# Kernel optimization log

Measured on AMD Instinct MI355X. Metric: run time of the kernel, lower is better.

Reference implementation:

```python
import jax, jax.numpy as jnp
import numpy as np

EPS = 1e-3    # Keras BatchNormalization default epsilon
ALPHA = 0.3   # Keras LeakyReLU default negative slope


def _bn(x, axes):
    # BatchNormalization(center=False, scale=False) in training mode: batch stats
    m = jnp.mean(x, axis=axes, keepdims=True)
    v = jnp.var(x, axis=axes, keepdims=True)
    return (x - m) * jax.lax.rsqrt(v + EPS)


def _leaky(x):
    return jnp.where(x > 0, x, ALPHA * x)


def setup_inputs() -> dict:
    key = jax.random.key(0)
    ks = jax.random.split(key, 8)
    B, A, D, Hid, H, hd = 8192, 16, 256, 512, 8, 64
    s = 0.02
    return {
        "state": jax.random.normal(ks[0], (B, A, D), jnp.float32),
        "agent_index": 3,
        "Ws": jax.random.normal(ks[1], (D, Hid), jnp.float32) * s,
        "bs": jnp.zeros((Hid,), jnp.float32),
        "Wc": jax.random.normal(ks[2], (D, Hid), jnp.float32) * s,
        "bc": jnp.zeros((Hid,), jnp.float32),
        "Wk": jax.random.normal(ks[3], (H, Hid, hd), jnp.float32) * s,
        "Wq": jax.random.normal(ks[4], (H, Hid, hd), jnp.float32) * s,
        "Wv": jax.random.normal(ks[5], (H, Hid, hd), jnp.float32) * s,
    }


def reference(state, agent_index, Ws, bs, Wc, bc, Wk, Wq, Wv):
    B = state.shape[0]
    H, _, hd = Wk.shape
    ai = int(agent_index)

    # current agent encoder: BN over batch, Dense, LeakyReLU -> [B, Hid]
    cur = state[:, ai, :]
    s_enc = _leaky(_bn(cur, (0,)) @ Ws + bs)

    # other agents encoder: BN over (batch, agent), Dense, LeakyReLU -> [B, A-1, Hid]
    others = jnp.concatenate([state[:, :ai, :], state[:, ai + 1:, :]], axis=1)
    sa_enc = _leaky(_bn(others, (0, 1)) @ Wc + bc)

    # batched per-head projections (replaces the python loop over heads)
    k = jnp.einsum('ban,hnd->bhad', sa_enc, Wk)           # [B,H,A-1,hd]
    v = _leaky(jnp.einsum('ban,hnd->bhad', sa_enc, Wv))   # [B,H,A-1,hd]
    q = jnp.einsum('bn,hnd->bhd', s_enc, Wq)              # [B,H,hd]

    scores = jnp.einsum('bhd,bhad->bha', q, k) / jnp.sqrt(jnp.float32(hd))
    w = jax.nn.softmax(scores, axis=-1)                   # [B,H,A-1]
    att = jnp.einsum('bha,bhad->bhd', w, v)               # [B,H,hd]

    # concat heads in order -> [B, H*hd]
    return att.reshape(B, H * hd)
```

## Files before the change

kernel.cpp:

```cpp
#include <hip/hip_runtime.h>
#include <hip/hip_bf16.h>

typedef __attribute__((ext_vector_type(8))) short short8;
typedef __attribute__((ext_vector_type(8))) unsigned short ushort8;
typedef __attribute__((ext_vector_type(4))) unsigned short bfu4;
typedef __attribute__((ext_vector_type(4))) float f32x4;

__device__ __forceinline__ unsigned short f2bf(float f){
  return __builtin_bit_cast(unsigned short, __float2bfloat16(f));
}
__device__ __forceinline__ float bf2f(unsigned short h){
  unsigned int u = ((unsigned int)h) << 16;
  return __builtin_bit_cast(float, u);
}
__device__ __forceinline__ float leaky(float x){ return x > 0.f ? x : 0.3f * x; }

__global__ __launch_bounds__(1024) void ca_stats_prep(const float* __restrict__ state,
    const int* __restrict__ agp, float* __restrict__ part, int B,
    const float* __restrict__ Wk, const float* __restrict__ Wv, const float* __restrict__ Wq,
    unsigned short* __restrict__ WkT, unsigned short* __restrict__ WvT,
    unsigned short* __restrict__ WqT, unsigned short* __restrict__ WkF2,
    unsigned short* __restrict__ WvF, unsigned short* __restrict__ WqF, int writeT){
  __shared__ f32x4 red[16][4][64];
  if (blockIdx.x < 256){
    int q = threadIdx.x & 63, sl = threadIdx.x >> 6;
    int ag = agp[0];
    int bPer = (B + 255) >> 8;
    int b0 = blockIdx.x * bPer;
    f32x4 zero4 = {0.f,0.f,0.f,0.f};
    f32x4 sC = zero4, ssC = zero4, sO = zero4, ssO = zero4;
    for (int b = sl; b < bPer; b += 16){
      int bb = b0 + b;
      if (bb >= B) continue;
      const float* row = state + ((size_t)bb << 12) + q*4;
      #pragma unroll
      for (int a = 0; a < 16; a++){
        f32x4 v = *(const f32x4*)(row + a*256);
        f32x4 vv = v * v;
        if (a == ag){ sC += v; ssC += vv; } else { sO += v; ssO += vv; }
      }
    }
    red[sl][0][q] = sC; red[sl][1][q] = ssC; red[sl][2][q] = sO; red[sl][3][q] = ssO;
    __syncthreads();
    if (threadIdx.x < 256){
      int st = threadIdx.x >> 6, qq = threadIdx.x & 63;
      f32x4 s = red[0][st][qq];
      #pragma unroll
      for (int g = 1; g < 16; g++) s += red[g][st][qq];
      *(f32x4*)(part + (size_t)blockIdx.x*1024 + st*256 + qq*4) = s;
    }
    return;
  }
  int bid2 = blockIdx.x - 256;
  int m = bid2 >> 8;
  int c = ((bid2 & 255) << 1) | (threadIdx.x >> 9);
  int n = threadIdx.x & 511;
  if (m == 3){
    size_t idx = (size_t)c*512 + n;
    int h = (int)(idx >> 15), nn = (int)((idx >> 6) & 511), dd = (int)(idx & 63);
    int nt = nn >> 4, j = nn & 15, kq = dd >> 5, hi = (dd >> 3) & 3, e = dd & 7;
    WkF2[(size_t)((h*32 + nt)*2 + kq)*512 + (hi*16 + j)*8 + e] = f2bf(Wk[idx]);
    return;
  }
  if (m == 0 && !writeT) return;
  int h = c >> 6, dd = c & 63;
  const float* W = (m == 0) ? Wk : (m == 1) ? Wv : Wq;
  unsigned short* O = (m == 0) ? WkT : (m == 1) ? WvT : WqT;
  float scale = (m == 2) ? 0.125f : 1.f;
  unsigned short v = f2bf(W[((size_t)h*512 + n)*64 + dd] * scale);
  if (m == 0 || writeT) O[(size_t)c*512 + n] = v;
  if (m != 0){
    int nt = (c >> 4) & 3, j = c & 15;
    int kk = n >> 5, hi = (n >> 3) & 3, e = n & 7;
    size_t fi = (size_t)((h*16 + kk)*4 + nt)*512 + (hi*16 + j)*8 + e;
    if (m == 1) WvF[fi] = v; else WqF[fi] = v;
  }
}

__global__ __launch_bounds__(1024) void ca_stats_final(const float* __restrict__ part,
    float* __restrict__ stats, int nblk, int B){
  int dl = threadIdx.x & 63, sl = threadIdx.x >> 6;
  int d = blockIdx.x*64 + dl;
  float sC = 0.f, ssC = 0.f, sO = 0.f, ssO = 0.f;
  for (int g = sl; g < nblk; g += 16){
    const float* p = part + (size_t)g * 1024;
    sC += p[d]; ssC += p[d+256]; sO += p[d+512]; ssO += p[d+768];
  }
  __shared__ float red[16][4][64];
  red[sl][0][dl] = sC; red[sl][1][dl] = ssC; red[sl][2][dl] = sO; red[sl][3][dl] = ssO;
  __syncthreads();
  if (sl == 0){
    sC = 0.f; ssC = 0.f; sO = 0.f; ssO = 0.f;
    #pragma unroll
    for (int g = 0; g < 16; g++){
      sC += red[g][0][dl]; ssC += red[g][1][dl]; sO += red[g][2][dl]; ssO += red[g][3][dl];
    }
    float nC = (float)B, nO = (float)B * 15.f;
    float mC = sC / nC, vC = ssC / nC - mC * mC;
    float mO = sO / nO, vO = ssO / nO - mO * mO;
    float rC = rsqrtf(vC + 1e-3f), rO = rsqrtf(vO + 1e-3f);
    stats[d] = rC; stats[d+256] = mC * rC; stats[d+512] = rO; stats[d+768] = mO * rO;
  }
}

__global__ __launch_bounds__(256) void ca_prep_sc(const float* __restrict__ Ws,
    const float* __restrict__ bs, const float* __restrict__ Wc, const float* __restrict__ bc,
    const float* __restrict__ stats, unsigned short* __restrict__ WsT,
    unsigned short* __restrict__ WcT, unsigned short* __restrict__ WsF,
    unsigned short* __restrict__ WcF, float* __restrict__ bsp, float* __restrict__ bcp,
    int writeT){
  int n = blockIdx.x, d = threadIdx.x;
  float rC = stats[d], mrC = stats[d+256], rO = stats[d+512], mrO = stats[d+768];
  float ws = Ws[(size_t)d*512 + n], wc = Wc[(size_t)d*512 + n];
  unsigned short wsb = f2bf(ws * rC), wcb = f2bf(wc * rO);
  if (writeT){
    WsT[(size_t)n*256 + d] = wsb;
    WcT[(size_t)n*256 + d] = wcb;
  }
  {
    int h = n >> 6, nt = (n >> 4) & 3, j = n & 15;
    int kk = d >> 5, hi = (d >> 3) & 3, e = d & 7;
    size_t fi = (size_t)((h*8 + kk)*4 + nt)*512 + (hi*16 + j)*8 + e;
    WsF[fi] = wsb;
    WcF[fi] = wcb;
  }
  __shared__ float red[256];
  red[d] = mrC * ws;
  __syncthreads();
  for (int s = 128; s > 0; s >>= 1){ if (d < s) red[d] += red[d+s]; __syncthreads(); }
  if (d == 0) bsp[n] = bs[n] - red[0];
  __syncthreads();
  red[d] = mrO * wc;
  __syncthreads();
  for (int s = 128; s > 0; s >>= 1){ if (d < s) red[d] += red[d+s]; __syncthreads(); }
  if (d == 0) bcp[n] = bc[n] - red[0];
}

__global__ __launch_bounds__(512) void ca_prep_kvq(const float* __restrict__ Wk,
    const float* __restrict__ Wv, const float* __restrict__ Wq,
    unsigned short* __restrict__ WkT, unsigned short* __restrict__ WvT,
    unsigned short* __restrict__ WqT){
  int c = blockIdx.x & 511, m = blockIdx.x >> 9;
  int n = threadIdx.x;
  int h = c >> 6, dd = c & 63;
  const float* W = (m == 0) ? Wk : (m == 1) ? Wv : Wq;
  unsigned short* O = (m == 0) ? WkT : (m == 1) ? WvT : WqT;
  float scale = (m == 2) ? 0.125f : 1.f;
  O[(size_t)c*512 + n] = f2bf(W[((size_t)h*512 + n)*64 + dd] * scale);
}

__global__ __launch_bounds__(512) void ca_q_kernel(const float* __restrict__ state,
    const int* __restrict__ agp,
    const unsigned short* __restrict__ WsT, const float* __restrict__ bsp,
    const unsigned short* __restrict__ WqT, unsigned short* __restrict__ Qws){
  __shared__ unsigned short U[32*512];
  __shared__ float bias_s[512];
  unsigned short* Alds = U;
  unsigned short* SE = U;
  int tid = threadIdx.x, lane = tid & 63, w = tid >> 6;
  int j = lane & 15, hi = lane >> 4;
  int b0 = blockIdx.x * 32;
  int ag = agp[0];

  for (int s = tid; s < 32*32; s += 512){
    int row = s >> 5, kg = s & 31;
    const float* p = state + (((size_t)(b0 + row) * 16 + ag) << 8) + kg * 8;
    f32x4 v0 = *(const f32x4*)p, v1 = *(const f32x4*)(p + 4);
    ushort8 hv;
    hv[0]=f2bf(v0[0]); hv[1]=f2bf(v0[1]); hv[2]=f2bf(v0[2]); hv[3]=f2bf(v0[3]);
    hv[4]=f2bf(v1[0]); hv[5]=f2bf(v1[1]); hv[6]=f2bf(v1[2]); hv[7]=f2bf(v1[3]);
    *(ushort8*)&Alds[row*256 + ((kg ^ (row & 7)) << 3)] = hv;
  }
  bias_s[tid & 511] = bsp[tid & 511];
  __syncthreads();

  int cb = w * 64;
  f32x4 zero4 = {0.f, 0.f, 0.f, 0.f};
  f32x4 acc[2][4];
  #pragma unroll
  for (int a1 = 0; a1 < 2; a1++)
    #pragma unroll
    for (int a2 = 0; a2 < 4; a2++) acc[a1][a2] = zero4;

  #pragma unroll
  for (int kk = 0; kk < 8; kk++){
    short8 bfr[4];
    #pragma unroll
    for (int nt = 0; nt < 4; nt++)
      bfr[nt] = *(const short8*)&WsT[(size_t)(cb + nt*16 + j)*256 + kk*32 + hi*8];
    #pragma unroll
    for (int mt = 0; mt < 2; mt++){
      int row = mt*16 + j;
      short8 afr = *(const short8*)&Alds[row*256 + ((((kk << 2) | hi) ^ (row & 7)) << 3)];
      #pragma unroll
      for (int nt = 0; nt < 4; nt++)
        acc[mt][nt] = __builtin_amdgcn_mfma_f32_16x16x32_bf16(afr, bfr[nt], acc[mt][nt], 0, 0, 0);
    }
  }
  __syncthreads();
  #pragma unroll
  for (int mt = 0; mt < 2; mt++)
    #pragma unroll
    for (int nt = 0; nt < 4; nt++)
      #pragma unroll
      for (int i = 0; i < 4; i++){
        int row = mt*16 + hi*4 + i, col = cb + nt*16 + j;
        float x = leaky(acc[mt][nt][i] + bias_s[col]);
        SE[row*512 + ((((col >> 3) ^ (row & 7)) << 3) | (col & 7))] = f2bf(x);
      }
  __syncthreads();

  f32x4 qa[2][4];
  #pragma unroll
  for (int a1 = 0; a1 < 2; a1++)
    #pragma unroll
    for (int a2 = 0; a2 < 4; a2++) qa[a1][a2] = zero4;
  #pragma unroll
  for (int kk = 0; kk < 16; kk++){
    short8 bfr[4];
    #pragma unroll
    for (int nt = 0; nt < 4; nt++)
      bfr[nt] = *(const short8*)&WqT[(size_t)(cb + nt*16 + j)*512 + kk*32 + hi*8];
    #pragma unroll
    for (int mt = 0; mt < 2; mt++){
      int row = mt*16 + j;
      short8 afr = *(const short8*)&SE[row*512 + ((((kk << 2) | hi) ^ (row & 7)) << 3)];
      #pragma unroll
      for (int nt = 0; nt < 4; nt++)
        qa[mt][nt] = __builtin_amdgcn_mfma_f32_16x16x32_bf16(afr, bfr[nt], qa[mt][nt], 0, 0, 0);
    }
  }
  #pragma unroll
  for (int mt = 0; mt < 2; mt++)
    #pragma unroll
    for (int nt = 0; nt < 4; nt++)
      #pragma unroll
      for (int i = 0; i < 4; i++)
        Qws[(size_t)(b0 + mt*16 + hi*4 + i)*512 + cb + nt*16 + j] = f2bf(qa[mt][nt][i]);
}

__global__ __launch_bounds__(1024) void ca_q_kernel_qk(const float* __restrict__ state,
    const int* __restrict__ agp,
    const unsigned short* __restrict__ WsF, const float* __restrict__ bsp,
    const unsigned short* __restrict__ WqF, const unsigned short* __restrict__ WkF2,
    unsigned short* __restrict__ QKws){
  __shared__ unsigned short U[2][16*512];
  __shared__ float bias_s[512];
  int tid = threadIdx.x, lane = tid & 63, w = tid >> 6;
  int g16 = w >> 3, wl = w & 7;
  int j = lane & 15, hi = lane >> 4;
  int b0 = blockIdx.x * 32 + g16 * 16;
  int ag = agp[0];
  f32x4 zero4 = {0.f, 0.f, 0.f, 0.f};
  unsigned short* Alds = U[g16];
  unsigned short* SE = U[g16];
  unsigned short* Qlds = U[g16];
  int sub = tid & 511;

  {
    int row = sub >> 5, kg = sub & 31;
    const float* p = state + (((size_t)(b0 + row) * 16 + ag) << 8) + kg * 8;
    f32x4 v0 = *(const f32x4*)p, v1 = *(const f32x4*)(p + 4);
    ushort8 hv;
    hv[0]=f2bf(v0[0]); hv[1]=f2bf(v0[1]); hv[2]=f2bf(v0[2]); hv[3]=f2bf(v0[3]);
    hv[4]=f2bf(v1[0]); hv[5]=f2bf(v1[1]); hv[6]=f2bf(v1[2]); hv[7]=f2bf(v1[3]);
    *(ushort8*)&Alds[row*256 + ((kg ^ (row & 7)) << 3)] = hv;
  }
  if (tid < 512) bias_s[tid] = bsp[tid];
  __syncthreads();

  int cb = wl * 64;

  f32x4 acc[4];
  #pragma unroll
  for (int a2 = 0; a2 < 4; a2++) acc[a2] = zero4;
  #pragma unroll
  for (int kk = 0; kk < 8; kk++){
    short8 bfr[4];
    #pragma unroll
    for (int nt = 0; nt < 4; nt++)
      bfr[nt] = *(const short8*)&WsF[(size_t)((wl*8 + kk)*4 + nt)*512 + lane*8];
    short8 afr = *(const short8*)&Alds[j*256 + ((((kk << 2) | hi) ^ (j & 7)) << 3)];
    #pragma unroll
    for (int nt = 0; nt < 4; nt++)
      acc[nt] = __builtin_amdgcn_mfma_f32_16x16x32_bf16(bfr[nt], afr, acc[nt], 0, 0, 0);
  }
  __syncthreads();
  #pragma unroll
  for (int nt = 0; nt < 4; nt++){
    int nb = cb + nt*16 + hi*4;
    int g = nb >> 3;
    bfu4 pk;
    #pragma unroll
    for (int i = 0; i < 4; i++) pk[i] = f2bf(leaky(acc[nt][i] + bias_s[nb + i]));
    *(bfu4*)&SE[j*512 + ((g ^ (j & 7)) << 3) + (hi & 1)*4] = pk;
  }
  __syncthreads();

  f32x4 qa[4];
  #pragma unroll
  for (int a2 = 0; a2 < 4; a2++) qa[a2] = zero4;
  #pragma unroll
  for (int kk = 0; kk < 16; kk++){
    short8 bfr[4];
    #pragma unroll
    for (int nt = 0; nt < 4; nt++)
      bfr[nt] = *(const short8*)&WqF[(size_t)((wl*16 + kk)*4 + nt)*512 + lane*8];
    short8 afr = *(const short8*)&SE[j*512 + ((((kk << 2) | hi) ^ (j & 7)) << 3)];
    #pragma unroll
    for (int nt = 0; nt < 4; nt++)
      qa[nt] = __builtin_amdgcn_mfma_f32_16x16x32_bf16(bfr[nt], afr, qa[nt], 0, 0, 0);
  }
  __syncthreads();
  #pragma unroll
  for (int nt = 0; nt < 4; nt++){
    int nb = cb + nt*16 + hi*4;
    int g = nb >> 3;
    bfu4 pk;
    #pragma unroll
    for (int i = 0; i < 4; i++) pk[i] = f2bf(qa[nt][i]);
    *(bfu4*)&Qlds[j*512 + ((g ^ (j & 7)) << 3) + (hi & 1)*4] = pk;
  }
  __syncthreads();

  short8 aq[2];
  #pragma unroll
  for (int kq = 0; kq < 2; kq++){
    int gq = wl*8 + kq*4 + hi;
    aq[kq] = *(const short8*)&Qlds[j*512 + ((gq ^ (j & 7)) << 3)];
  }
  for (int nt = 0; nt < 32; nt++){
    short8 bf0 = *(const short8*)&WkF2[(size_t)((wl*32 + nt)*2 + 0)*512 + lane*8];
    short8 bf1 = *(const short8*)&WkF2[(size_t)((wl*32 + nt)*2 + 1)*512 + lane*8];
    f32x4 qt = zero4;
    qt = __builtin_amdgcn_mfma_f32_16x16x32_bf16(bf0, aq[0], qt, 0, 0, 0);
    qt = __builtin_amdgcn_mfma_f32_16x16x32_bf16(bf1, aq[1], qt, 0, 0, 0);
    bfu4 pk;
    pk[0] = f2bf(qt[0]); pk[1] = f2bf(qt[1]); pk[2] = f2bf(qt[2]); pk[3] = f2bf(qt[3]);
    *(bfu4*)&QKws[((size_t)(b0 + j)*8 + wl)*512 + nt*16 + hi*4] = pk;
  }
}

__global__ __launch_bounds__(512) void ca_main_kernel_qk(const float* __restrict__ state,
    const int* __restrict__ agp,
    const unsigned short* __restrict__ WcF, const float* __restrict__ bcp,
    const unsigned short* __restrict__ WvF, const unsigned short* __restrict__ QKws,
    float* __restrict__ out){
  __shared__ unsigned short U[128*512];
  __shared__ float bias_s[512];
  __shared__ float Wl[8*16*8];
  unsigned short* Alds = U;
  unsigned short* SA = U;
  int tid = threadIdx.x, lane = tid & 63, w = tid >> 6;
  int j = lane & 15, hi = lane >> 4;
  int b0 = blockIdx.x * 8;
  int ag = agp[0];
  f32x4 zero4 = {0.f, 0.f, 0.f, 0.f};
  short8 zero8 = {0,0,0,0,0,0,0,0};

  #pragma unroll
  for (int g = 0; g < 2; g++){
    f32x4 st0[4], st1[4];
    #pragma unroll
    for (int it = 0; it < 4; it++){
      int s = tid + 512*(g*4 + it);
      int row = s >> 5, kg = s & 31;
      int bl = row >> 4, ai = row & 15;
      if (ai < 15){
        int a = ai + (ai >= ag ? 1 : 0);
        const float* p = state + (((size_t)(b0 + bl) * 16 + a) << 8) + kg * 8;
        st0[it] = *(const f32x4*)p;
        st1[it] = *(const f32x4*)(p + 4);
      } else { st0[it] = zero4; st1[it] = zero4; }
    }
    #pragma unroll
    for (int it = 0; it < 4; it++){
      int s = tid + 512*(g*4 + it);
      int row = s >> 5, kg = s & 31;
      ushort8 hv;
      hv[0]=f2bf(st0[it][0]); hv[1]=f2bf(st0[it][1]); hv[2]=f2bf(st0[it][2]); hv[3]=f2bf(st0[it][3]);
      hv[4]=f2bf(st1[it][0]); hv[5]=f2bf(st1[it][1]); hv[6]=f2bf(st1[it][2]); hv[7]=f2bf(st1[it][3]);
      *(ushort8*)&Alds[row*256 + ((kg ^ (row & 7)) << 3)] = hv;
    }
  }
  bias_s[tid] = bcp[tid];
  __syncthreads();

  int cb = w * 64;

  f32x4 acc[8][4];
  #pragma unroll
  for (int a1 = 0; a1 < 8; a1++)
    #pragma unroll
    for (int a2 = 0; a2 < 4; a2++) acc[a1][a2] = zero4;
  {
    short8 bcur[4], bnxt[4];
    #pragma unroll
    for (int nt = 0; nt < 4; nt++)
      bcur[nt] = *(const short8*)&WcF[(size_t)((w*8 + 0)*4 + nt)*512 + lane*8];
    #pragma unroll 2
    for (int kk = 0; kk < 8; kk++){
      if (kk < 7){
        #pragma unroll
        for (int nt = 0; nt < 4; nt++)
          bnxt[nt] = *(const short8*)&WcF[(size_t)((w*8 + kk + 1)*4 + nt)*512 + lane*8];
      }
      #pragma unroll
      for (int mt = 0; mt < 8; mt++){
        int row = mt*16 + j;
        short8 afr = *(const short8*)&Alds[row*256 + ((((kk << 2) | hi) ^ (row & 7)) << 3)];
        #pragma unroll
        for (int nt = 0; nt < 4; nt++)
          acc[mt][nt] = __builtin_amdgcn_mfma_f32_16x16x32_bf16(bcur[nt], afr, acc[mt][nt], 0, 0, 0);
      }
      #pragma unroll
      for (int nt = 0; nt < 4; nt++) bcur[nt] = bnxt[nt];
    }
  }
  __syncthreads();
  #pragma unroll
  for (int mt = 0; mt < 8; mt++)
    #pragma unroll
    for (int nt = 0; nt < 4; nt++){
      int m = mt*16 + j;
      int nb = cb + nt*16 + hi*4;
      int g = nb >> 3;
      bfu4 pk;
      #pragma unroll
      for (int i = 0; i < 4; i++) pk[i] = f2bf(leaky(acc[mt][nt][i] + bias_s[nb + i]));
      *(bfu4*)&SA[m*512 + ((g ^ (m & 7)) << 3) + (hi & 1)*4] = pk;
    }
  __syncthreads();

  f32x4 qs = zero4;
  {
    size_t qbase = ((size_t)(b0 + w)*8 + (j & 7))*512;
    #pragma unroll
    for (int kk = 0; kk < 16; kk++){
      short8 bq = *(const short8*)&QKws[qbase + kk*32 + hi*8];
      if (j >= 8) bq = zero8;
      int row = w*16 + j;
      short8 afr = *(const short8*)&SA[row*512 + ((((kk << 2) | hi) ^ (row & 7)) << 3)];
      qs = __builtin_amdgcn_mfma_f32_16x16x32_bf16(afr, bq, qs, 0, 0, 0);
    }
  }
  {
    float sv0 = qs[0], sv1 = qs[1], sv2 = qs[2], sv3 = qs[3];
    sv3 = (hi == 3) ? -1e30f : sv3;
    float m = fmaxf(fmaxf(sv0, sv1), fmaxf(sv2, sv3));
    m = fmaxf(m, __shfl_xor(m, 16)); m = fmaxf(m, __shfl_xor(m, 32));
    float e0 = __expf(sv0-m), e1 = __expf(sv1-m), e2 = __expf(sv2-m), e3 = __expf(sv3-m);
    float sum = e0 + e1 + e2 + e3;
    sum += __shfl_xor(sum, 16); sum += __shfl_xor(sum, 32);
    float inv = 1.f / sum;
    if (j < 8){
      Wl[w*128 + (hi*4+0)*8 + j] = e0*inv;
      Wl[w*128 + (hi*4+1)*8 + j] = e1*inv;
      Wl[w*128 + (hi*4+2)*8 + j] = e2*inv;
      Wl[w*128 + (hi*4+3)*8 + j] = e3*inv;
    }
  }

  f32x4 va[8][4];
  #pragma unroll
  for (int a1 = 0; a1 < 8; a1++)
    #pragma unroll
    for (int a2 = 0; a2 < 4; a2++) va[a1][a2] = zero4;
  {
    short8 bcur[4], bnxt[4];
    #pragma unroll
    for (int nt = 0; nt < 4; nt++)
      bcur[nt] = *(const short8*)&WvF[(size_t)((w*16 + 0)*4 + nt)*512 + lane*8];
    #pragma unroll 2
    for (int kk = 0; kk < 16; kk++){
      if (kk < 15){
        #pragma unroll
        for (int nt = 0; nt < 4; nt++)
          bnxt[nt] = *(const short8*)&WvF[(size_t)((w*16 + kk + 1)*4 + nt)*512 + lane*8];
      }
      #pragma unroll
      for (int mt = 0; mt < 8; mt++){
        int row = mt*16 + j;
        short8 afr = *(const short8*)&SA[row*512 + ((((kk << 2) | hi) ^ (row & 7)) << 3)];
        #pragma unroll
        for (int nt = 0; nt < 4; nt++)
          va[mt][nt] = __builtin_amdgcn_mfma_f32_16x16x32_bf16(afr, bcur[nt], va[mt][nt], 0, 0, 0);
      }
      #pragma unroll
      for (int nt = 0; nt < 4; nt++) bcur[nt] = bnxt[nt];
    }
  }
  __syncthreads();

  #pragma unroll
  for (int mt = 0; mt < 8; mt++){
    float w0 = Wl[mt*128 + (hi*4+0)*8 + w];
    float w1 = Wl[mt*128 + (hi*4+1)*8 + w];
    float w2 = Wl[mt*128 + (hi*4+2)*8 + w];
    float w3 = Wl[mt*128 + (hi*4+3)*8 + w];
    float ap0 = w0*leaky(va[mt][0][0]) + w1*leaky(va[mt][0][1]) + w2*leaky(va[mt][0][2]) + w3*leaky(va[mt][0][3]);
    float ap1 = w0*leaky(va[mt][1][0]) + w1*leaky(va[mt][1][1]) + w2*leaky(va[mt][1][2]) + w3*leaky(va[mt][1][3]);
    float ap2 = w0*leaky(va[mt][2][0]) + w1*leaky(va[mt][2][1]) + w2*leaky(va[mt][2][2]) + w3*leaky(va[mt][2][3]);
    float ap3 = w0*leaky(va[mt][3][0]) + w1*leaky(va[mt][3][1]) + w2*leaky(va[mt][3][2]) + w3*leaky(va[mt][3][3]);
    ap0 += __shfl_xor(ap0, 16); ap0 += __shfl_xor(ap0, 32);
    ap1 += __shfl_xor(ap1, 16); ap1 += __shfl_xor(ap1, 32);
    ap2 += __shfl_xor(ap2, 16); ap2 += __shfl_xor(ap2, 32);
    ap3 += __shfl_xor(ap3, 16); ap3 += __shfl_xor(ap3, 32);
    float val = (hi == 0) ? ap0 : (hi == 1) ? ap1 : (hi == 2) ? ap2 : ap3;
    out[(size_t)(b0 + mt)*512 + cb + lane] = val;
  }
}

__global__ __launch_bounds__(512) void ca_main_kernel(const float* __restrict__ state,
    const int* __restrict__ agp,
    const unsigned short* __restrict__ WcT, const float* __restrict__ bcp,
    const unsigned short* __restrict__ WkT, const unsigned short* __restrict__ WvT,
    const unsigned short* __restrict__ Qws, float* __restrict__ out){
  __shared__ unsigned short U[128*512];
  __shared__ unsigned short Qs[8*512];
  __shared__ float bias_s[512];
  unsigned short* Alds = U;
  unsigned short* SA = U;
  int tid = threadIdx.x, lane = tid & 63, w = tid >> 6;
  int j = lane & 15, hi = lane >> 4;
  int b0 = blockIdx.x * 8;
  int ag = agp[0];
  f32x4 zero4 = {0.f, 0.f, 0.f, 0.f};

  #pragma unroll
  for (int g = 0; g < 2; g++){
    f32x4 st0[4], st1[4];
    #pragma unroll
    for (int it = 0; it < 4; it++){
      int s = tid + 512*(g*4 + it);
      int row = s >> 5, kg = s & 31;
      int bl = row >> 4, ai = row & 15;
      if (ai < 15){
        int a = ai + (ai >= ag ? 1 : 0);
        const float* p = state + (((size_t)(b0 + bl) * 16 + a) << 8) + kg * 8;
        st0[it] = *(const f32x4*)p;
        st1[it] = *(const f32x4*)(p + 4);
      } else { st0[it] = zero4; st1[it] = zero4; }
    }
    #pragma unroll
    for (int it = 0; it < 4; it++){
      int s = tid + 512*(g*4 + it);
      int row = s >> 5, kg = s & 31;
      ushort8 hv;
      hv[0]=f2bf(st0[it][0]); hv[1]=f2bf(st0[it][1]); hv[2]=f2bf(st0[it][2]); hv[3]=f2bf(st0[it][3]);
      hv[4]=f2bf(st1[it][0]); hv[5]=f2bf(st1[it][1]); hv[6]=f2bf(st1[it][2]); hv[7]=f2bf(st1[it][3]);
      *(ushort8*)&Alds[row*256 + ((kg ^ (row & 7)) << 3)] = hv;
    }
  }
  *(ushort8*)&Qs[tid*8] = *(const ushort8*)&Qws[(size_t)b0*512 + tid*8];
  bias_s[tid] = bcp[tid];
  __syncthreads();

  int cb = w * 64;

  f32x4 acc[8][4];
  #pragma unroll
  for (int a1 = 0; a1 < 8; a1++)
    #pragma unroll
    for (int a2 = 0; a2 < 4; a2++) acc[a1][a2] = zero4;
  {
    short8 bcur[4], bnxt[4];
    #pragma unroll
    for (int nt = 0; nt < 4; nt++)
      bcur[nt] = *(const short8*)&WcT[(size_t)(cb + nt*16 + j)*256 + hi*8];
    #pragma unroll 1
    for (int kk = 0; kk < 8; kk++){
      if (kk < 7){
        #pragma unroll
        for (int nt = 0; nt < 4; nt++)
          bnxt[nt] = *(const short8*)&WcT[(size_t)(cb + nt*16 + j)*256 + (kk+1)*32 + hi*8];
      }
      #pragma unroll
      for (int mt = 0; mt < 8; mt++){
        int row = mt*16 + j;
        short8 afr = *(const short8*)&Alds[row*256 + ((((kk << 2) | hi) ^ (row & 7)) << 3)];
        #pragma unroll
        for (int nt = 0; nt < 4; nt++)
          acc[mt][nt] = __builtin_amdgcn_mfma_f32_16x16x32_bf16(afr, bcur[nt], acc[mt][nt], 0, 0, 0);
      }
      #pragma unroll
      for (int nt = 0; nt < 4; nt++) bcur[nt] = bnxt[nt];
    }
  }
  __syncthreads();
  #pragma unroll
  for (int mt = 0; mt < 8; mt++)
    #pragma unroll
    for (int nt = 0; nt < 4; nt++)
      #pragma unroll
      for (int i = 0; i < 4; i++){
        int row = mt*16 + hi*4 + i, col = cb + nt*16 + j;
        float x = leaky(acc[mt][nt][i] + bias_s[col]);
        SA[row*512 + ((((col >> 3) ^ (row & 7)) << 3) | (col & 7))] = f2bf(x);
      }
  __syncthreads();

  f32x4 ka[8][4];
  #pragma unroll
  for (int a1 = 0; a1 < 8; a1++)
    #pragma unroll
    for (int a2 = 0; a2 < 4; a2++) ka[a1][a2] = zero4;
  {
    short8 bcur[4], bnxt[4];
    #pragma unroll
    for (int nt = 0; nt < 4; nt++)
      bcur[nt] = *(const short8*)&WkT[(size_t)(cb + nt*16 + j)*512 + hi*8];
    #pragma unroll 1
    for (int kk = 0; kk < 16; kk++){
      if (kk < 15){
        #pragma unroll
        for (int nt = 0; nt < 4; nt++)
          bnxt[nt] = *(const short8*)&WkT[(size_t)(cb + nt*16 + j)*512 + (kk+1)*32 + hi*8];
      }
      #pragma unroll
      for (int mt = 0; mt < 8; mt++){
        int row = mt*16 + j;
        short8 afr = *(const short8*)&SA[row*512 + ((((kk << 2) | hi) ^ (row & 7)) << 3)];
        #pragma unroll
        for (int nt = 0; nt < 4; nt++)
          ka[mt][nt] = __builtin_amdgcn_mfma_f32_16x16x32_bf16(afr, bcur[nt], ka[mt][nt], 0, 0, 0);
      }
      #pragma unroll
      for (int nt = 0; nt < 4; nt++) bcur[nt] = bnxt[nt];
    }
  }

  float wgt[8][4];
  #pragma unroll
  for (int mt = 0; mt < 8; mt++){
    float sv[4];
    #pragma unroll
    for (int i = 0; i < 4; i++){
      float t = 0.f;
      #pragma unroll
      for (int nt = 0; nt < 4; nt++)
        t += bf2f(Qs[mt*512 + cb + nt*16 + j]) * ka[mt][nt][i];
      t += __shfl_xor(t, 1); t += __shfl_xor(t, 2);
      t += __shfl_xor(t, 4); t += __shfl_xor(t, 8);
      sv[i] = t;
    }
    sv[3] = (hi == 3) ? -1e30f : sv[3];
    float m = fmaxf(fmaxf(sv[0], sv[1]), fmaxf(sv[2], sv[3]));
    m = fmaxf(m, __shfl_xor(m, 16)); m = fmaxf(m, __shfl_xor(m, 32));
    float e0 = __expf(sv[0]-m), e1 = __expf(sv[1]-m), e2 = __expf(sv[2]-m), e3 = __expf(sv[3]-m);
    float sum = e0 + e1 + e2 + e3;
    sum += __shfl_xor(sum, 16); sum += __shfl_xor(sum, 32);
    float inv = 1.f / sum;
    wgt[mt][0] = e0*inv; wgt[mt][1] = e1*inv; wgt[mt][2] = e2*inv; wgt[mt][3] = e3*inv;
  }

  f32x4 va[8][4];
  #pragma unroll
  for (int a1 = 0; a1 < 8; a1++)
    #pragma unroll
    for (int a2 = 0; a2 < 4; a2++) va[a1][a2] = zero4;
  {
    short8 bcur[4], bnxt[4];
    #pragma unroll
    for (int nt = 0; nt < 4; nt++)
      bcur[nt] = *(const short8*)&WvT[(size_t)(cb + nt*16 + j)*512 + hi*8];
    #pragma unroll 1
    for (int kk = 0; kk < 16; kk++){
      if (kk < 15){
        #pragma unroll
        for (int nt = 0; nt < 4; nt++)
          bnxt[nt] = *(const short8*)&WvT[(size_t)(cb + nt*16 + j)*512 + (kk+1)*32 + hi*8];
      }
      #pragma unroll
      for (int mt = 0; mt < 8; mt++){
        int row = mt*16 + j;
        short8 afr = *(const short8*)&SA[row*512 + ((((kk << 2) | hi) ^ (row & 7)) << 3)];
        #pragma unroll
        for (int nt = 0; nt < 4; nt++)
          va[mt][nt] = __builtin_amdgcn_mfma_f32_16x16x32_bf16(afr, bcur[nt], va[mt][nt], 0, 0, 0);
      }
      #pragma unroll
      for (int nt = 0; nt < 4; nt++) bcur[nt] = bnxt[nt];
    }
  }

  #pragma unroll
  for (int mt = 0; mt < 8; mt++){
    float ap0 = 0.f, ap1 = 0.f, ap2 = 0.f, ap3 = 0.f;
    #pragma unroll
    for (int i = 0; i < 4; i++){
      float wv = wgt[mt][i];
      ap0 += wv * leaky(va[mt][0][i]);
      ap1 += wv * leaky(va[mt][1][i]);
      ap2 += wv * leaky(va[mt][2][i]);
      ap3 += wv * leaky(va[mt][3][i]);
    }
    ap0 += __shfl_xor(ap0, 16); ap0 += __shfl_xor(ap0, 32);
    ap1 += __shfl_xor(ap1, 16); ap1 += __shfl_xor(ap1, 32);
    ap2 += __shfl_xor(ap2, 16); ap2 += __shfl_xor(ap2, 32);
    ap3 += __shfl_xor(ap3, 16); ap3 += __shfl_xor(ap3, 32);
    float val = (hi == 0) ? ap0 : (hi == 1) ? ap1 : (hi == 2) ? ap2 : ap3;
    out[(size_t)(b0 + mt)*512 + cb + lane] = val;
  }
}

extern "C" void kernel_launch(void* const* d_in, const int* in_sizes, int n_in,
                              void* d_out, int out_size, void* d_ws, size_t ws_size,
                              hipStream_t stream) {
  const float* state = (const float*)d_in[0];
  const int*   agp   = (const int*)d_in[1];
  const float* Ws    = (const float*)d_in[2];
  const float* bs    = (const float*)d_in[3];
  const float* Wc    = (const float*)d_in[4];
  const float* bc    = (const float*)d_in[5];
  const float* Wk    = (const float*)d_in[6];
  const float* Wq    = (const float*)d_in[7];
  const float* Wv    = (const float*)d_in[8];
  float* out = (float*)d_out;
  int B = in_sizes[0] / 4096;

  char* wsb = (char*)d_ws;
  float* part  = (float*)wsb;
  float* stats = (float*)(wsb + (1 << 20));
  float* bsp   = (float*)(wsb + (1 << 20) + 4096);
  float* bcp   = (float*)(wsb + (1 << 20) + 6144);
  unsigned short* WsT  = (unsigned short*)(wsb + (1 << 20) + 8192);
  unsigned short* WcT  = WsT  + 512*256;
  unsigned short* WkT  = WcT  + 512*256;
  unsigned short* WvT  = WkT  + 512*512;
  unsigned short* WqT  = WvT  + 512*512;
  unsigned short* WkF2 = WqT  + 512*512;
  unsigned short* Qws  = WkF2 + 512*512;
  unsigned short* QKws = Qws  + (size_t)B*512;
  unsigned short* WsF  = Qws;
  unsigned short* WcF  = WsF + 512*256;
  unsigned short* WqF  = WcF + 512*256;
  unsigned short* WvF  = WqF + 512*512;

  size_t need = ((size_t)(1 << 20) + 8192)
              + 2ull*(512*256 + 512*256 + 512*512 + 512*512 + 512*512 + 512*512)
              + 2ull*B*512 + 2ull*B*8*512;
  bool qkp = (ws_size >= need);
  int writeT = qkp ? 0 : 1;

  hipLaunchKernelGGL(ca_stats_prep, dim3(1280), dim3(1024), 0, stream, state, agp, part, B,
                     Wk, Wv, Wq, WkT, WvT, WqT, WkF2, WvF, WqF, writeT);
  hipLaunchKernelGGL(ca_stats_final, dim3(4), dim3(1024), 0, stream, part, stats, 256, B);
  hipLaunchKernelGGL(ca_prep_sc,     dim3(512), dim3(256), 0, stream, Ws, bs, Wc, bc, stats, WsT, WcT, WsF, WcF, bsp, bcp, writeT);
  if (qkp){
    hipLaunchKernelGGL(ca_q_kernel_qk,   dim3(B/32),dim3(1024), 0, stream, state, agp, WsF, bsp, WqF, WkF2, QKws);
    hipLaunchKernelGGL(ca_main_kernel_qk,dim3(B/8), dim3(512), 0, stream, state, agp, WcF, bcp, WvF, QKws, out);
  } else {
    hipLaunchKernelGGL(ca_prep_kvq,      dim3(1536),dim3(512), 0, stream, Wk, Wv, Wq, WkT, WvT, WqT);
    hipLaunchKernelGGL(ca_q_kernel,      dim3(B/32),dim3(512), 0, stream, state, agp, WsT, bsp, WqT, Qws);
    hipLaunchKernelGGL(ca_main_kernel,   dim3(B/8), dim3(512), 0, stream, state, agp, WcT, bcp, WkT, WvT, Qws, out);
  }
}
```

Baseline: 215.1 us.

## Apply batch-norm on activations in consumers and drop weight-folding prep launch

Batch-norm is no longer folded into the Ws/Wc weights and biases by a separate prep kernel. The q and main kernels now normalize state rows in registers from the stats buffer while converting to bf16, and use the raw biases. Packing Ws/Wc into the fragment layout moves into the stats kernel's spare blocks, so it runs alongside the reduction and one dependent launch leaves the fast path. The main kernel also loads its QK fragments before the barrier to hide global latency. The cost is a few extra FMAs per loaded element and bf16 rounding applied to the normalized inputs rather than to the folded weights.

```diff
diff --git a/kernel.cpp b/kernel.cpp
--- a/kernel.cpp
+++ b/kernel.cpp
@@ -18,9 +18,10 @@
 __global__ __launch_bounds__(1024) void ca_stats_prep(const float* __restrict__ state,
     const int* __restrict__ agp, float* __restrict__ part, int B,
     const float* __restrict__ Wk, const float* __restrict__ Wv, const float* __restrict__ Wq,
-    unsigned short* __restrict__ WkT, unsigned short* __restrict__ WvT,
-    unsigned short* __restrict__ WqT, unsigned short* __restrict__ WkF2,
-    unsigned short* __restrict__ WvF, unsigned short* __restrict__ WqF, int writeT){
+    const float* __restrict__ Ws, const float* __restrict__ Wc,
+    unsigned short* __restrict__ WkF2, unsigned short* __restrict__ WvF,
+    unsigned short* __restrict__ WqF, unsigned short* __restrict__ WsF,
+    unsigned short* __restrict__ WcF){
   __shared__ f32x4 red[16][4][64];
   if (blockIdx.x < 256){
     int q = threadIdx.x & 63, sl = threadIdx.x >> 6;
@@ -53,28 +54,34 @@
   }
   int bid2 = blockIdx.x - 256;
   int m = bid2 >> 8;
+  if (m == 3){
+    int item = ((bid2 & 255) << 10) | threadIdx.x;
+    const float* W = (item < 131072) ? Ws : Wc;
+    unsigned short* O = (item < 131072) ? WsF : WcF;
+    int it2 = item & 131071;
+    int n = it2 >> 8, d = it2 & 255;
+    int h = n >> 6, nt = (n >> 4) & 3, j = n & 15;
+    int kk = d >> 5, hi = (d >> 3) & 3, e = d & 7;
+    O[(size_t)((h*8 + kk)*4 + nt)*512 + (hi*16 + j)*8 + e] = f2bf(W[(size_t)d*512 + n]);
+    return;
+  }
   int c = ((bid2 & 255) << 1) | (threadIdx.x >> 9);
   int n = threadIdx.x & 511;
-  if (m == 3){
+  if (m == 2){
     size_t idx = (size_t)c*512 + n;
     int h = (int)(idx >> 15), nn = (int)((idx >> 6) & 511), dd = (int)(idx & 63);
     int nt = nn >> 4, j = nn & 15, kq = dd >> 5, hi = (dd >> 3) & 3, e = dd & 7;
     WkF2[(size_t)((h*32 + nt)*2 + kq)*512 + (hi*16 + j)*8 + e] = f2bf(Wk[idx]);
     return;
   }
-  if (m == 0 && !writeT) return;
   int h = c >> 6, dd = c & 63;
-  const float* W = (m == 0) ? Wk : (m == 1) ? Wv : Wq;
-  unsigned short* O = (m == 0) ? WkT : (m == 1) ? WvT : WqT;
-  float scale = (m == 2) ? 0.125f : 1.f;
+  const float* W = (m == 0) ? Wv : Wq;
+  float scale = (m == 1) ? 0.125f : 1.f;
   unsigned short v = f2bf(W[((size_t)h*512 + n)*64 + dd] * scale);
-  if (m == 0 || writeT) O[(size_t)c*512 + n] = v;
-  if (m != 0){
-    int nt = (c >> 4) & 3, j = c & 15;
-    int kk = n >> 5, hi = (n >> 3) & 3, e = n & 7;
-    size_t fi = (size_t)((h*16 + kk)*4 + nt)*512 + (hi*16 + j)*8 + e;
-    if (m == 1) WvF[fi] = v; else WqF[fi] = v;
-  }
+  int nt = (c >> 4) & 3, j = c & 15;
+  int kk = n >> 5, hi = (n >> 3) & 3, e = n & 7;
+  size_t fi = (size_t)((h*16 + kk)*4 + nt)*512 + (hi*16 + j)*8 + e;
+  if (m == 0) WvF[fi] = v; else WqF[fi] = v;
 }
 
 __global__ __launch_bounds__(1024) void ca_stats_final(const float* __restrict__ part,
@@ -106,24 +113,12 @@
 __global__ __launch_bounds__(256) void ca_prep_sc(const float* __restrict__ Ws,
     const float* __restrict__ bs, const float* __restrict__ Wc, const float* __restrict__ bc,
     const float* __restrict__ stats, unsigned short* __restrict__ WsT,
-    unsigned short* __restrict__ WcT, unsigned short* __restrict__ WsF,
-    unsigned short* __restrict__ WcF, float* __restrict__ bsp, float* __restrict__ bcp,
-    int writeT){
+    unsigned short* __restrict__ WcT, float* __restrict__ bsp, float* __restrict__ bcp){
   int n = blockIdx.x, d = threadIdx.x;
   float rC = stats[d], mrC = stats[d+256], rO = stats[d+512], mrO = stats[d+768];
   float ws = Ws[(size_t)d*512 + n], wc = Wc[(size_t)d*512 + n];
-  unsigned short wsb = f2bf(ws * rC), wcb = f2bf(wc * rO);
-  if (writeT){
-    WsT[(size_t)n*256 + d] = wsb;
-    WcT[(size_t)n*256 + d] = wcb;
-  }
-  {
-    int h = n >> 6, nt = (n >> 4) & 3, j = n & 15;
-    int kk = d >> 5, hi = (d >> 3) & 3, e = d & 7;
-    size_t fi = (size_t)((h*8 + kk)*4 + nt)*512 + (hi*16 + j)*8 + e;
-    WsF[fi] = wsb;
-    WcF[fi] = wcb;
-  }
+  WsT[(size_t)n*256 + d] = f2bf(ws * rC);
+  WcT[(size_t)n*256 + d] = f2bf(wc * rO);
   __shared__ float red[256];
   red[d] = mrC * ws;
   __syncthreads();
@@ -240,8 +235,8 @@
 }
 
 __global__ __launch_bounds__(1024) void ca_q_kernel_qk(const float* __restrict__ state,
-    const int* __restrict__ agp,
-    const unsigned short* __restrict__ WsF, const float* __restrict__ bsp,
+    const int* __restrict__ agp, const float* __restrict__ stats,
+    const float* __restrict__ bs, const unsigned short* __restrict__ WsF,
     const unsigned short* __restrict__ WqF, const unsigned short* __restrict__ WkF2,
     unsigned short* __restrict__ QKws){
   __shared__ unsigned short U[2][16*512];
@@ -259,14 +254,21 @@
 
   {
     int row = sub >> 5, kg = sub & 31;
-    const float* p = state + (((size_t)(b0 + row) * 16 + ag) << 8) + kg * 8;
+    int kg0 = kg * 8;
+    f32x4 rc0 = *(const f32x4*)(stats + kg0);
+    f32x4 rc1 = *(const f32x4*)(stats + kg0 + 4);
+    f32x4 mr0 = *(const f32x4*)(stats + 256 + kg0);
+    f32x4 mr1 = *(const f32x4*)(stats + 256 + kg0 + 4);
+    const float* p = state + (((size_t)(b0 + row) * 16 + ag) << 8) + kg0;
     f32x4 v0 = *(const f32x4*)p, v1 = *(const f32x4*)(p + 4);
+    v0 = v0 * rc0 - mr0;
+    v1 = v1 * rc1 - mr1;
     ushort8 hv;
     hv[0]=f2bf(v0[0]); hv[1]=f2bf(v0[1]); hv[2]=f2bf(v0[2]); hv[3]=f2bf(v0[3]);
     hv[4]=f2bf(v1[0]); hv[5]=f2bf(v1[1]); hv[6]=f2bf(v1[2]); hv[7]=f2bf(v1[3]);
     *(ushort8*)&Alds[row*256 + ((kg ^ (row & 7)) << 3)] = hv;
   }
-  if (tid < 512) bias_s[tid] = bsp[tid];
+  if (tid < 512) bias_s[tid] = bs[tid];
   __syncthreads();
 
   int cb = wl * 64;
@@ -342,8 +344,8 @@
 }
 
 __global__ __launch_bounds__(512) void ca_main_kernel_qk(const float* __restrict__ state,
-    const int* __restrict__ agp,
-    const unsigned short* __restrict__ WcF, const float* __restrict__ bcp,
+    const int* __restrict__ agp, const float* __restrict__ stats,
+    const unsigned short* __restrict__ WcF, const float* __restrict__ bc,
     const unsigned short* __restrict__ WvF, const unsigned short* __restrict__ QKws,
     float* __restrict__ out){
   __shared__ unsigned short U[128*512];
@@ -358,32 +360,44 @@
   f32x4 zero4 = {0.f, 0.f, 0.f, 0.f};
   short8 zero8 = {0,0,0,0,0,0,0,0};
 
-  #pragma unroll
-  for (int g = 0; g < 2; g++){
-    f32x4 st0[4], st1[4];
-    #pragma unroll
-    for (int it = 0; it < 4; it++){
-      int s = tid + 512*(g*4 + it);
-      int row = s >> 5, kg = s & 31;
-      int bl = row >> 4, ai = row & 15;
-      if (ai < 15){
-        int a = ai + (ai >= ag ? 1 : 0);
-        const float* p = state + (((size_t)(b0 + bl) * 16 + a) << 8) + kg * 8;
-        st0[it] = *(const f32x4*)p;
-        st1[it] = *(const f32x4*)(p + 4);
-      } else { st0[it] = zero4; st1[it] = zero4; }
-    }
-    #pragma unroll
-    for (int it = 0; it < 4; it++){
-      int s = tid + 512*(g*4 + it);
-      int row = s >> 5, kg = s & 31;
-      ushort8 hv;
-      hv[0]=f2bf(st0[it][0]); hv[1]=f2bf(st0[it][1]); hv[2]=f2bf(st0[it][2]); hv[3]=f2bf(st0[it][3]);
-      hv[4]=f2bf(st1[it][0]); hv[5]=f2bf(st1[it][1]); hv[6]=f2bf(st1[it][2]); hv[7]=f2bf(st1[it][3]);
-      *(ushort8*)&Alds[row*256 + ((kg ^ (row & 7)) << 3)] = hv;
-    }
-  }
-  bias_s[tid] = bcp[tid];
+  {
+    int kg0 = (tid & 31) * 8;
+    f32x4 rc0 = *(const f32x4*)(stats + 512 + kg0);
+    f32x4 rc1 = *(const f32x4*)(stats + 512 + kg0 + 4);
+    f32x4 mr0 = *(const f32x4*)(stats + 768 + kg0);
+    f32x4 mr1 = *(const f32x4*)(stats + 768 + kg0 + 4);
+    #pragma unroll
+    for (int g = 0; g < 2; g++){
+      f32x4 st0[4], st1[4];
+      #pragma unroll
+      for (int it = 0; it < 4; it++){
+        int s = tid + 512*(g*4 + it);
+        int row = s >> 5;
+        int bl = row >> 4, ai = row & 15;
+        if (ai < 15){
+          int a = ai + (ai >= ag ? 1 : 0);
+          const float* p = state + (((size_t)(b0 + bl) * 16 + a) << 8) + kg0;
+          st0[it] = *(const f32x4*)p;
+          st1[it] = *(const f32x4*)(p + 4);
+        } else { st0[it] = zero4; st1[it] = zero4; }
+      }
+      #pragma unroll
+      for (int it = 0; it < 4; it++){
+        int s = tid + 512*(g*4 + it);
+        int row = s >> 5, kg = s & 31;
+        int ai = row & 15;
+        ushort8 hv = {0,0,0,0,0,0,0,0};
+        if (ai < 15){
+          f32x4 v0 = st0[it] * rc0 - mr0;
+          f32x4 v1 = st1[it] * rc1 - mr1;
+          hv[0]=f2bf(v0[0]); hv[1]=f2bf(v0[1]); hv[2]=f2bf(v0[2]); hv[3]=f2bf(v0[3]);
+          hv[4]=f2bf(v1[0]); hv[5]=f2bf(v1[1]); hv[6]=f2bf(v1[2]); hv[7]=f2bf(v1[3]);
+        }
+        *(ushort8*)&Alds[row*256 + ((kg ^ (row & 7)) << 3)] = hv;
+      }
+    }
+  }
+  bias_s[tid] = bc[tid];
   __syncthreads();
 
   int cb = w * 64;
@@ -416,6 +430,13 @@
       #pragma unroll
       for (int nt = 0; nt < 4; nt++) bcur[nt] = bnxt[nt];
     }
+  }
+  short8 bq[16];
+  {
+    size_t qbase = ((size_t)(b0 + w)*8 + (j & 7))*512;
+    #pragma unroll
+    for (int kk = 0; kk < 16; kk++)
+      bq[kk] = *(const short8*)&QKws[qbase + kk*32 + hi*8];
   }
   __syncthreads();
   #pragma unroll
@@ -433,16 +454,12 @@
   __syncthreads();
 
   f32x4 qs = zero4;
-  {
-    size_t qbase = ((size_t)(b0 + w)*8 + (j & 7))*512;
-    #pragma unroll
-    for (int kk = 0; kk < 16; kk++){
-      short8 bq = *(const short8*)&QKws[qbase + kk*32 + hi*8];
-      if (j >= 8) bq = zero8;
-      int row = w*16 + j;
-      short8 afr = *(const short8*)&SA[row*512 + ((((kk << 2) | hi) ^ (row & 7)) << 3)];
-      qs = __builtin_amdgcn_mfma_f32_16x16x32_bf16(afr, bq, qs, 0, 0, 0);
-    }
+  #pragma unroll
+  for (int kk = 0; kk < 16; kk++){
+    short8 bqv = (j < 8) ? bq[kk] : zero8;
+    int row = w*16 + j;
+    short8 afr = *(const short8*)&SA[row*512 + ((((kk << 2) | hi) ^ (row & 7)) << 3)];
+    qs = __builtin_amdgcn_mfma_f32_16x16x32_bf16(afr, bqv, qs, 0, 0, 0);
   }
   {
     float sv0 = qs[0], sv1 = qs[1], sv2 = qs[2], sv3 = qs[3];
@@ -741,16 +758,15 @@
               + 2ull*(512*256 + 512*256 + 512*512 + 512*512 + 512*512 + 512*512)
               + 2ull*B*512 + 2ull*B*8*512;
   bool qkp = (ws_size >= need);
-  int writeT = qkp ? 0 : 1;
 
   hipLaunchKernelGGL(ca_stats_prep, dim3(1280), dim3(1024), 0, stream, state, agp, part, B,
-                     Wk, Wv, Wq, WkT, WvT, WqT, WkF2, WvF, WqF, writeT);
+                     Wk, Wv, Wq, Ws, Wc, WkF2, WvF, WqF, WsF, WcF);
   hipLaunchKernelGGL(ca_stats_final, dim3(4), dim3(1024), 0, stream, part, stats, 256, B);
-  hipLaunchKernelGGL(ca_prep_sc,     dim3(512), dim3(256), 0, stream, Ws, bs, Wc, bc, stats, WsT, WcT, WsF, WcF, bsp, bcp, writeT);
   if (qkp){
-    hipLaunchKernelGGL(ca_q_kernel_qk,   dim3(B/32),dim3(1024), 0, stream, state, agp, WsF, bsp, WqF, WkF2, QKws);
-    hipLaunchKernelGGL(ca_main_kernel_qk,dim3(B/8), dim3(512), 0, stream, state, agp, WcF, bcp, WvF, QKws, out);
+    hipLaunchKernelGGL(ca_q_kernel_qk,   dim3(B/32),dim3(1024), 0, stream, state, agp, stats, bs, WsF, WqF, WkF2, QKws);
+    hipLaunchKernelGGL(ca_main_kernel_qk,dim3(B/8), dim3(512), 0, stream, state, agp, stats, WcF, bc, WvF, QKws, out);
   } else {
+    hipLaunchKernelGGL(ca_prep_sc,       dim3(512), dim3(256), 0, stream, Ws, bs, Wc, bc, stats, WsT, WcT, bsp, bcp);
     hipLaunchKernelGGL(ca_prep_kvq,      dim3(1536),dim3(512), 0, stream, Wk, Wv, Wq, WkT, WvT, WqT);
     hipLaunchKernelGGL(ca_q_kernel,      dim3(B/32),dim3(512), 0, stream, state, agp, WsT, bsp, WqT, Qws);
     hipLaunchKernelGGL(ca_main_kernel,   dim3(B/8), dim3(512), 0, stream, state, agp, WcT, bcp, WkT, WvT, Qws, out);
```

Measured after the change: 207.6 us. -3.5%, faster.
